# Optimization experiments

Measured on AMD Instinct MI355X. Metric: run time of the kernel, lower is better.

The kernel has to match this reference:

```python
import math
import numpy as np
import jax, jax.numpy as jnp

C = 8  # hidden multiplicity (num_channels)
B, N = 4, 4096

# ---------- real Wigner 3j (e3nn convention: Frobenius norm 1) ----------

def _su2_cg(l1, l2, l3):
    f = math.factorial
    def cg(m1, m2, m3):
        if m1 + m2 != m3:
            return 0.0
        pref = math.sqrt((2 * l3 + 1) * f(l3 + l1 - l2) * f(l3 - l1 + l2) * f(l1 + l2 - l3) / f(l1 + l2 + l3 + 1))
        pref *= math.sqrt(f(l3 + m3) * f(l3 - m3) * f(l1 - m1) * f(l1 + m1) * f(l2 - m2) * f(l2 + m2))
        s = 0.0
        for k in range(l1 + l2 - l3 + 1):
            d = [k, l1 + l2 - l3 - k, l1 - m1 - k, l2 + m2 - k, l3 - l2 + m1 + k, l3 - l1 - m2 + k]
            if min(d) < 0:
                continue
            s += (-1.0) ** k / np.prod([float(f(x)) for x in d])
        return pref * s
    out = np.zeros((2 * l1 + 1, 2 * l2 + 1, 2 * l3 + 1))
    for i, m1 in enumerate(range(-l1, l1 + 1)):
        for j, m2 in enumerate(range(-l2, l2 + 1)):
            for k, m3 in enumerate(range(-l3, l3 + 1)):
                out[i, j, k] = cg(m1, m2, m3)
    return out

def _q_real_to_complex(l):
    q = np.zeros((2 * l + 1, 2 * l + 1), dtype=np.complex128)
    rs2 = 1.0 / math.sqrt(2.0)
    for m in range(-l, 0):
        q[l + m, l + abs(m)] = rs2
        q[l + m, l - abs(m)] = -1j * rs2
    q[l, l] = 1.0
    for m in range(1, l + 1):
        q[l + m, l + abs(m)] = (-1) ** m * rs2
        q[l + m, l - abs(m)] = 1j * (-1) ** m * rs2
    return (-1j) ** l * q

def _w3j(l1, l2, l3):
    Q1, Q2, Q3 = _q_real_to_complex(l1), _q_real_to_complex(l2), _q_real_to_complex(l3)
    Cc = _su2_cg(l1, l2, l3).astype(np.complex128)
    Cr = np.real(np.einsum('ij,kl,mn,ikm->jln', Q1, Q2, np.conj(Q3), Cc))
    return (Cr / np.linalg.norm(Cr)).astype(np.float32)

# tensor-product paths (selection rules for 4e/6e inputs, 0e/2e SH, 4e/6e outputs)
VAL_PATHS = [(4, 0, 4), (4, 2, 4), (6, 2, 4), (4, 2, 6), (6, 0, 6), (6, 2, 6)]
OUT_PATHS = [(4, 4, 4), (4, 6, 4), (6, 4, 4), (6, 6, 4), (4, 4, 6), (4, 6, 6), (6, 4, 6), (6, 6, 6)]
# path normalization ('element'): fan-in = 3*C for tp_val outputs, 4*C^2 for tp_out outputs
W3J_VAL = [jnp.asarray(_w3j(*p) * math.sqrt((2 * p[2] + 1) / (3.0 * C))) for p in VAL_PATHS]
W3J_OUT = [jnp.asarray(_w3j(*p) * math.sqrt((2 * p[2] + 1) / (4.0 * C * C))) for p in OUT_PATHS]


def _forward(feat, sh_lr, log_s, pos_w, pos_b, w_lin_in, w_val, w_out, w_lin_out):
    b, n, _ = feat.shape
    f4, f6 = feat[..., :9], feat[..., 9:]                      # 1x4e, 1x6e
    f4n = f4 / jnp.maximum(jnp.linalg.norm(f4, axis=-1, keepdims=True), 1e-12)
    f6n = f6 / jnp.maximum(jnp.linalg.norm(f6, axis=-1, keepdims=True), 1e-12)
    s4, s6 = jnp.exp(log_s[0]), jnp.exp(log_s[1])
    scores = s4 * jnp.einsum('bnd,bmd->bnm', f4n, f4n) + s6 * jnp.einsum('bnd,bmd->bnm', f6n, f6n)
    pb = sh_lr @ pos_w + pos_b                                 # (N,)
    scores = scores + (pb[:, None] + pb[None, :])[None]
    attn = jax.nn.softmax(scores.astype(jnp.float32), axis=-1).astype(feat.dtype)

    h4 = f4[:, :, None, :] * w_lin_in[0][None, None, :, None]  # (B,N,C,9)
    h6 = f6[:, :, None, :] * w_lin_in[1][None, None, :, None]  # (B,N,C,13)

    y = {0: sh_lr[:, :1], 2: sh_lr[:, 1:]}                     # (N,1), (N,5)
    hx = {4: h4, 6: h6}
    v = {4: jnp.zeros((b, n, C, 9), feat.dtype), 6: jnp.zeros((b, n, C, 13), feat.dtype)}
    for p, (l1, l2, l3) in enumerate(VAL_PATHS):
        v[l3] = v[l3] + jnp.einsum('bnui,nj,ijk,uw->bnwk', hx[l1], y[l2], W3J_VAL[p], w_val[p])
    vals = jnp.concatenate([v[4].reshape(b, n, 9 * C), v[6].reshape(b, n, 13 * C)], axis=-1)

    ctx = jnp.einsum('bnm,bmd->bnd', attn, vals)               # (B,N,22C)
    cx = {4: ctx[..., :9 * C].reshape(b, n, C, 9), 6: ctx[..., 9 * C:].reshape(b, n, C, 13)}
    o = {4: jnp.zeros((b, n, C, 9), feat.dtype), 6: jnp.zeros((b, n, C, 13), feat.dtype)}
    for p, (l1, l2, l3) in enumerate(OUT_PATHS):
        o[l3] = o[l3] + jnp.einsum('bnui,bnvj,ijk,uvw->bnwk', hx[l1], cx[l2], W3J_OUT[p], w_out[p])

    inv_sc = 1.0 / math.sqrt(C)                                # lin_out fan_in = C
    d4 = jnp.einsum('bnui,u->bni', o[4], w_lin_out[0]) * inv_sc
    d6 = jnp.einsum('bnui,u->bni', o[6], w_lin_out[1]) * inv_sc
    return jnp.concatenate([d4, d6], axis=-1)                  # (B,N,22)


def setup_inputs() -> dict:
    key = jax.random.key(0)
    ks = jax.random.split(key, 8)
    feat = jax.random.normal(ks[0], (B, N, 22), jnp.float32)
    sh_lr = jax.random.normal(ks[1], (N, 6), jnp.float32)
    log_s = jnp.array([math.log(1.0 / 3.0), math.log(1.0 / math.sqrt(13.0))], jnp.float32)
    pos_w = 0.01 * jax.random.normal(ks[2], (6,), jnp.float32)
    pos_b = jnp.zeros((), jnp.float32)
    w_lin_in = jax.random.normal(ks[3], (2, C), jnp.float32)
    w_val = jax.random.normal(ks[4], (6, C, C), jnp.float32)
    w_out = jax.random.normal(ks[5], (8, C, C, C), jnp.float32)
    w_lin_out = jax.random.normal(ks[6], (2, C), jnp.float32)
    return dict(feat=feat, sh_lr=sh_lr, log_s=log_s, pos_w=pos_w, pos_b=pos_b,
                w_lin_in=w_lin_in, w_val=w_val, w_out=w_out, w_lin_out=w_lin_out)


def reference(feat, sh_lr, log_s, pos_w, pos_b, w_lin_in, w_val, w_out, w_lin_out):
    return _forward(feat, sh_lr, log_s, pos_w, pos_b, w_lin_in, w_val, w_out, w_lin_out)
```

## Files before the change

kernel.cpp:

```cpp
#include <hip/hip_runtime.h>
#include <cmath>

#define NN 4096
#define BB 4
#define CCH 8

#define OFF_W3JVAL 0
#define OFF_W3JOUT 2688
#define OFF_CTX0   13568
#define CTXS       1572864
#define OFFB_KGH   25220096ULL
#define OFFB_KGL   26268672ULL
#define OFFB_VG    27317248ULL
#define OFFB_WBH   30462976ULL
#define OFFB_WBL   30493696ULL

typedef short s16x8 __attribute__((ext_vector_type(8)));
typedef _Float16 f16x8 __attribute__((ext_vector_type(8)));
typedef float f32x4 __attribute__((ext_vector_type(4)));
typedef unsigned int u32x4 __attribute__((ext_vector_type(4)));
typedef unsigned int u32x2 __attribute__((ext_vector_type(2)));

static __device__ __forceinline__ unsigned short f2bf(float x){
  unsigned u = __float_as_uint(x);
  return (unsigned short)((u + 0x7FFFu + ((u >> 16) & 1u)) >> 16);
}
static __device__ __forceinline__ float bf2f(unsigned short h){
  return __uint_as_float(((unsigned)h) << 16);
}
static __device__ __forceinline__ unsigned pk2r(float v){
  unsigned short h = f2bf(v);
  unsigned short l = f2bf(v - bf2f(h));
  return ((unsigned)l << 16) | (unsigned)h;
}
static __device__ __forceinline__ unsigned short f2h(float x){
  return __builtin_bit_cast(unsigned short, (_Float16)x);
}
static __device__ __forceinline__ void unpk(u32x4 a, u32x4 b, s16x8& h, s16x8& l){
  u32x4 hw = { __builtin_amdgcn_perm(a[1],a[0],0x05040100u),
               __builtin_amdgcn_perm(a[3],a[2],0x05040100u),
               __builtin_amdgcn_perm(b[1],b[0],0x05040100u),
               __builtin_amdgcn_perm(b[3],b[2],0x05040100u)};
  u32x4 lw = { __builtin_amdgcn_perm(a[1],a[0],0x07060302u),
               __builtin_amdgcn_perm(a[3],a[2],0x07060302u),
               __builtin_amdgcn_perm(b[1],b[0],0x07060302u),
               __builtin_amdgcn_perm(b[3],b[2],0x07060302u)};
  h = __builtin_bit_cast(s16x8, hw);
  l = __builtin_bit_cast(s16x8, lw);
}
static __device__ __forceinline__ void barrier_lds(){
  __asm__ volatile("s_waitcnt lgkmcnt(0)\n\ts_barrier" ::: "memory");
}

static __device__ __forceinline__ void qentf(int l, int r, int c, float& re, float& im){
  re=0.f; im=0.f;
  float s = ((l&3)==2)? -1.f : 1.f;
  const float rs2 = 0.70710678118654752440f;
  if(r < l){
    if(c == 2*l - r) re = s*rs2;
    else if(c == r)  im = -s*rs2;
  } else if(r == l){
    if(c == l) re = s;
  } else {
    float sg = ((r-l)&1)? -1.f : 1.f;
    if(c == r) re = s*sg*rs2;
    else if(c == 2*l - r) im = s*sg*rs2;
  }
}
__global__ __launch_bounds__(256) void k_tab(float* __restrict__ Wv, float* __restrict__ Wo){
  __shared__ float Ccf[2197];
  __shared__ float red[256];
  __shared__ double factS[20];
  int t = threadIdx.x;
  int p = blockIdx.x;
  if(t==0){
    double f=1.0; factS[0]=1.0;
    for(int i=1;i<20;i++){ f*=(double)i; factS[i]=f; }
  }
  const int L1[14]={4,4,6,4,6,6, 4,4,6,6,4,4,6,6};
  const int L2[14]={0,2,2,2,0,2, 4,6,4,6,4,6,4,6};
  const int L3[14]={4,4,4,6,6,6, 4,4,4,4,6,6,6,6};
  const int OFF[14]={0,81,486,1071,1656,1825, 0,729,1782,2835,4356,5409,6930,8451};
  int l1=L1[p], l2=L2[p], l3=L3[p];
  int d1=2*l1+1, d2=2*l2+1, d3=2*l3+1;
  int tot = d1*d2*d3;
  float* dst = (p<6) ? (Wv+OFF[p]) : (Wo+OFF[p]);
  float scale = (p<6) ? sqrtf((2.f*l3+1.f)/24.f) : sqrtf((2.f*l3+1.f)/256.f);
  __syncthreads();
  #pragma unroll 1
  for(int e=t; e<tot; e+=256){
    int i = e/(d2*d3), rem = e - i*(d2*d3), j = rem/d3, k = rem - j*d3;
    int m1=i-l1, m2=j-l2, m3=k-l3;
    double v=0.0;
    if(m1+m2==m3){
      double pref = sqrt((2.0*l3+1.0)*factS[l3+l1-l2]*factS[l3-l1+l2]*factS[l1+l2-l3]/factS[l1+l2+l3+1]);
      pref *= sqrt(factS[l3+m3]*factS[l3-m3]*factS[l1-m1]*factS[l1+m1]*factS[l2-m2]*factS[l2+m2]);
      double s=0.0;
      #pragma unroll 1
      for(int kk=0; kk<=l1+l2-l3; kk++){
        int dd0=kk, dd1=l1+l2-l3-kk, dd2=l1-m1-kk, dd3=l2+m2-kk, dd4=l3-l2+m1+kk, dd5=l3-l1-m2+kk;
        int mn=dd0;
        if(dd1<mn)mn=dd1; if(dd2<mn)mn=dd2; if(dd3<mn)mn=dd3; if(dd4<mn)mn=dd4; if(dd5<mn)mn=dd5;
        if(mn<0) continue;
        double prod = factS[dd0]*factS[dd1]*factS[dd2]*factS[dd3]*factS[dd4]*factS[dd5];
        s += ((kk&1)? -1.0:1.0)/prod;
      }
      v = pref*s;
    }
    Ccf[e]=(float)v;
  }
  __syncthreads();
  float nacc=0.f;
  #pragma unroll 1
  for(int e=t; e<tot; e+=256){
    int j = e/(d2*d3), rem = e - j*(d2*d3), l = rem/d3, n = rem - l*d3;
    float re = 0.f;
    #pragma unroll
    for(int ii=0; ii<2; ii++){
      int i = ii ? (2*l1 - j) : j;
      float q1r,q1i; qentf(l1,i,j,q1r,q1i);
      if(ii && i==j){ q1r=0.f; q1i=0.f; }
      #pragma unroll
      for(int kk=0; kk<2; kk++){
        int k = kk ? (2*l2 - l) : l;
        float q2r,q2i; qentf(l2,k,l,q2r,q2i);
        if(kk && k==l){ q2r=0.f; q2i=0.f; }
        float ar = q1r*q2r - q1i*q2i;
        float ai = q1r*q2i + q1i*q2r;
        #pragma unroll
        for(int mm=0; mm<2; mm++){
          int m = mm ? (2*l3 - n) : n;
          float q3r,q3i; qentf(l3,m,n,q3r,q3i);
          if(mm && m==n){ q3r=0.f; q3i=0.f; }
          float coef = ar*q3r + ai*q3i;
          re = fmaf(coef, Ccf[(i*d2+k)*d3+m], re);
        }
      }
    }
    dst[e]=re;
    nacc = fmaf(re,re,nacc);
  }
  red[t]=nacc;
  __syncthreads();
  #pragma unroll 1
  for(int s=128;s>0;s>>=1){
    if(t<s) red[t]+=red[t+s];
    __syncthreads();
  }
  float c = scale/sqrtf(red[0]);
  #pragma unroll 1
  for(int e=t; e<tot; e+=256) dst[e]*=c;
}

__global__ void k_weights(const float* __restrict__ wli, const float* __restrict__ wval,
                          const float* __restrict__ wout, const float* __restrict__ wlo,
                          const float* __restrict__ Wv,
                          unsigned short* __restrict__ WBH, unsigned short* __restrict__ WBL){
  __shared__ float bws[48];
  __shared__ float scs[64];
  __shared__ float As[24];
  int t = threadIdx.x;
  if(t<48){
    const int val_l1[6]={0,0,1,0,1,1};
    int p=t>>3, w=t&7;
    float s=0.f;
    for(int u=0;u<8;u++) s = fmaf(wli[val_l1[p]*8+u], wval[(p*8+u)*8+w], s);
    bws[t]=s;
  }
  {
    const int out_l1[8]={0,0,1,1,0,0,1,1};
    const int out_l3[8]={0,0,0,0,1,1,1,1};
    int p=t>>3, v=t&7;
    float s=0.f;
    for(int u=0;u<8;u++){
      float a=wli[out_l1[p]*8+u];
      for(int w=0;w<8;w++) s = fmaf(wout[((p*8+u)*8+v)*8+w]*a, wlo[out_l3[p]*8+w], s);
    }
    scs[t]=s*0.35355339059327373f;
  }
  __syncthreads();
  if(t<24){
    int p=t/3, i3=t-3*p;
    int vp = (p&1)*3 + i3;
    float s=0.f;
    for(int w=0;w<8;w++) s = fmaf(scs[p*8+w], bws[vp*8+w], s);
    As[t]=s;
  }
  __syncthreads();
  int base = blockIdx.x*960;
  for(int k=0;k<15;k++){
    int cell = base + k*64 + t;
    int f = cell/160, c = cell - f*160;
    float v = 0.f;
    if(f < 88 && c < 132){
      int seg = f/22, off = f - seg*22;
      int even = (off < 9);
      int p = 2*seg + (even?0:1);
      int jo = even ? off : off-9;
      int l1, i, jj;
      if(c < 54){ l1=4; i=c/6; jj=c-6*i; }
      else { int cc=c-54; l1=6; i=cc/6; jj=cc-6*i; }
      if(even){
        if(l1==4 && jj==0)      v = As[p*3+0]*Wv[i*9+jo];
        else if(l1==4)          v = As[p*3+1]*Wv[81+(i*5+jj-1)*9+jo];
        else if(jj>=1)          v = As[p*3+2]*Wv[486+(i*5+jj-1)*9+jo];
      } else {
        if(l1==4 && jj>=1)      v = As[p*3+0]*Wv[1071+(i*5+jj-1)*13+jo];
        else if(l1==6 && jj==0) v = As[p*3+1]*Wv[1656+i*13+jo];
        else if(l1==6)          v = As[p*3+2]*Wv[1825+(i*5+jj-1)*13+jo];
      }
    } else if(f==88 && c==132){
      v = 1.0f;
    }
    unsigned short h = f2bf(v);
    WBH[cell] = h;
    WBL[cell] = f2bf(v - bf2f(h));
  }
}

__launch_bounds__(128)
__global__ void k_prep(const float* __restrict__ feat, const float* __restrict__ sh,
                       const float* __restrict__ log_s, const float* __restrict__ pos_w,
                       const float* __restrict__ pos_b,
                       const unsigned short* __restrict__ WBH,
                       const unsigned short* __restrict__ WBL,
                       unsigned short* __restrict__ Kgh, unsigned short* __restrict__ Kgl,
                       unsigned short* __restrict__ Vg){
  __shared__ __align__(16) unsigned int Pbuf[16*164];
  __shared__ unsigned int Po[96*17];
  __shared__ float epbs[16];
  int tid = threadIdx.x;
  int w2 = tid >> 6, lane = tid & 63;
  int lm = lane & 15, quad = lane >> 4;
  int seg = w2*4 + quad;
  int panel = blockIdx.x >> 2, mt = blockIdx.x & 3;
  int idxp = panel*64 + mt*16 + lm;
  int n = idxp & (NN-1);
  const float* fp = feat + (size_t)idxp*22;
  const float* shp = sh + n*6;
  float f[22];
  #pragma unroll
  for(int c=0;c<22;c++) f[c]=fp[c];
  float y[6];
  #pragma unroll
  for(int j=0;j<6;j++) y[j]=shp[j];
  if(tid<16){
    float pb = pos_b[0];
    #pragma unroll
    for(int j=0;j<6;j++) pb = fmaf(y[j], pos_w[j], pb);
    epbs[lm] = __expf(pb);
    float n4=0.f, n6=0.f;
    #pragma unroll
    for(int c=0;c<9;c++) n4 += f[c]*f[c];
    #pragma unroll
    for(int c=9;c<22;c++) n6 += f[c]*f[c];
    n4 = fmaxf(sqrtf(n4), 1e-12f);
    n6 = fmaxf(sqrtf(n6), 1e-12f);
    float s4 = __expf(log_s[0]), s6 = __expf(log_s[1]);
    float a4 = sqrtf(s4)/n4, a6 = sqrtf(s6)/n6;
    unsigned short* kph = Kgh + (size_t)idxp*32;
    unsigned short* kpl = Kgl + (size_t)idxp*32;
    #pragma unroll
    for(int c=0;c<22;c++){
      float qv = f[c] * (c<9 ? a4 : a6);
      unsigned short h = f2bf(qv);
      kph[c]=h; kpl[c]=f2bf(qv - bf2f(h));
    }
    #pragma unroll
    for(int c=22;c<32;c++){ kph[c]=0; kpl[c]=0; }
  }
  #pragma unroll
  for(int j4=0;j4<5;j4++){
    u32x4 wv;
    #pragma unroll
    for(int e=0;e<4;e++){
      int c = seg*20 + j4*4 + e;
      float pv;
      if(c<54){ int i=c/6, jj=c-6*i; pv = f[i]*y[jj]; }
      else if(c<132){ int cc=c-54; int i=cc/6, jj=cc-6*i; pv = f[9+i]*y[jj]; }
      else if(c==132) pv = 1.0f;
      else pv = 0.0f;
      wv[e] = pk2r(pv);
    }
    *(u32x4*)&Pbuf[lm*164 + seg*20 + j4*4] = wv;
  }
  __syncthreads();
  f32x4 acc[3];
  #pragma unroll
  for(int ft=0;ft<3;ft++)
    #pragma unroll
    for(int i=0;i<4;i++) acc[ft][i]=0.f;
  for(int kc=0;kc<5;kc++){
    const u32x4* ap = (const u32x4*)&Pbuf[lm*164 + kc*32 + quad*8];
    s16x8 Ah, Al;
    unpk(ap[0], ap[1], Ah, Al);
    #pragma unroll
    for(int ft=0;ft<3;ft++){
      int ftg = w2*3 + ft;
      size_t bo = (size_t)(ftg*16+lm)*160 + kc*32 + quad*8;
      s16x8 Bh = *(const s16x8*)(WBH + bo);
      s16x8 Bl = *(const s16x8*)(WBL + bo);
      f32x4 a = acc[ft];
      a = __builtin_amdgcn_mfma_f32_16x16x32_bf16(Al, Bl, a, 0,0,0);
      a = __builtin_amdgcn_mfma_f32_16x16x32_bf16(Al, Bh, a, 0,0,0);
      a = __builtin_amdgcn_mfma_f32_16x16x32_bf16(Ah, Bl, a, 0,0,0);
      a = __builtin_amdgcn_mfma_f32_16x16x32_bf16(Ah, Bh, a, 0,0,0);
      acc[ft] = a;
    }
  }
  #pragma unroll
  for(int r=0;r<4;r++){
    float e = epbs[quad*4 + r];
    #pragma unroll
    for(int ft=0;ft<3;ft++){
      int ftg = w2*3 + ft;
      Po[(ftg*16+lm)*17 + quad*4 + r] = (unsigned)f2h(acc[ft][r]*e);
    }
  }
  __syncthreads();
  unsigned int* vO32 = (unsigned int*)(Vg + (size_t)panel*96*64);
  #pragma unroll
  for(int wv=0; wv<6; wv++){
    int idx2 = wv*128 + tid;
    int g = idx2 >> 3, j = idx2 & 7;
    unsigned lo = Po[g*17 + 2*j] & 0xFFFFu;
    unsigned hi = Po[g*17 + 2*j + 1] & 0xFFFFu;
    vO32[g*32 + mt*8 + j] = lo | (hi<<16);
  }
}

#define ESB 16384
__global__ __launch_bounds__(512)
__attribute__((amdgpu_waves_per_eu(4, 4)))
void k_attn(const unsigned short* __restrict__ Kgh,
            const unsigned short* __restrict__ Kgl,
            const unsigned short* __restrict__ Vg,
            float* __restrict__ ctx0){
  __shared__ __align__(16) unsigned char Es[2][ESB];
  int tid = threadIdx.x;
  int lane = tid & 63, w = tid >> 6;
  int lm = lane & 15, quad = lane >> 4;
  int blk = blockIdx.x;
  int b = blk & 3, hd = (blk>>2)&3, qb = blk >> 4;
  int qrow0 = qb * 128;
  const unsigned short* KhB = Kgh + (size_t)b*NN*32;
  const unsigned short* KlB = Kgl + (size_t)b*NN*32;
  const unsigned short* VB  = Vg  + (size_t)b*64*96*64;
  float* ctx = ctx0 + (size_t)hd*CTXS + (size_t)b*NN*96;

  int sq = w & 3;
  int sk = w >> 2;

  s16x8 qh[2], ql[2];
  #pragma unroll
  for(int q2=0;q2<2;q2++){
    size_t ro = (size_t)(qrow0 + (2*sq+q2)*16 + lm)*32 + (size_t)quad*8;
    qh[q2] = *(const s16x8*)(KhB + ro);
    ql[q2] = *(const s16x8*)(KlB + ro);
  }
  int wofs[2][2], rofs[2][2];
  #pragma unroll
  for(int q2=0;q2<2;q2++){
    int row = (2*sq+q2)*16 + lm;
    int xo = (row & 7) << 4;
    #pragma unroll
    for(int k2=0;k2<2;k2++)
      wofs[k2][q2] = row*128 + ((((2*sk+k2)*32) + quad*8) ^ xo);
    #pragma unroll
    for(int ks=0;ks<2;ks++)
      rofs[ks][q2] = row*128 + (((ks*64) + quad*16) ^ xo);
  }

  f32x4 acc[2][3];
  #pragma unroll
  for(int q2=0;q2<2;q2++)
    #pragma unroll
    for(int ft=0;ft<3;ft++)
      #pragma unroll
      for(int i=0;i<4;i++) acc[q2][ft][i]=0.f;

  s16x8 kh_[2][2], kl_[2][2];
  f16x8 vv[2][3];

#define MFB(A,Bv,C) __builtin_amdgcn_mfma_f32_16x16x32_bf16(A,Bv,C,0,0,0)
#define MFH(A,Bv,C) __builtin_amdgcn_mfma_f32_16x16x32_f16(A,Bv,C,0,0,0)

#define LOADK(T,Bk) { size_t pk_ = (size_t)(hd*16+(T))*2048; \
  _Pragma("unroll") \
  for(int k2=0;k2<2;k2++){ \
    size_t ko_ = pk_ + (size_t)((2*sk+k2)*16+lm)*32 + (size_t)(quad*8); \
    kh_[Bk][k2] = *(const s16x8*)(KhB + ko_); \
    kl_[Bk][k2] = *(const s16x8*)(KlB + ko_); } }

#define LOADV(T) { size_t pv_ = (size_t)(hd*16+(T))*6144; \
  _Pragma("unroll") \
  for(int ks=0;ks<2;ks++) \
  _Pragma("unroll") \
  for(int ft=0;ft<3;ft++){ \
    size_t vo_ = pv_ + (size_t)((3*sk+ft)*16+lm)*64 + (size_t)(ks*32+quad*8); \
    vv[ks][ft] = *(const f16x8*)(VB + vo_); } }

#define SPH(Bk,CUR) { \
  _Pragma("unroll") \
  for(int k2=0;k2<2;k2++) \
  _Pragma("unroll") \
  for(int q2=0;q2<2;q2++){ \
    f32x4 s_ = {0.f,0.f,0.f,0.f}; \
    s_ = MFB(kl_[Bk][k2], qh[q2], s_); \
    s_ = MFB(kh_[Bk][k2], ql[q2], s_); \
    s_ = MFB(kh_[Bk][k2], qh[q2], s_); \
    unsigned u01_ = (unsigned)f2h(__expf(s_[0])) | ((unsigned)f2h(__expf(s_[1]))<<16); \
    unsigned u23_ = (unsigned)f2h(__expf(s_[2])) | ((unsigned)f2h(__expf(s_[3]))<<16); \
    *(u32x2*)&Es[CUR][wofs[k2][q2]] = (u32x2){u01_, u23_}; } }

#define PVH(PRV) { \
  _Pragma("unroll") \
  for(int ks=0;ks<2;ks++) \
  _Pragma("unroll") \
  for(int q2=0;q2<2;q2++){ \
    f16x8 e_ = *(const f16x8*)&Es[PRV][rofs[ks][q2]]; \
    _Pragma("unroll") \
    for(int ft=0;ft<3;ft++) \
      acc[q2][ft] = MFH(e_, vv[ks][ft], acc[q2][ft]); } }

  LOADK(0,0);
  LOADV(0);
  LOADK(1,1);
  SPH(0,0);
  barrier_lds();

  #pragma unroll 1
  for(int t=1; t<14; t+=2){
    LOADK(t+1,0);
    PVH(0);
    LOADV(t);
    SPH(1,1);
    barrier_lds();
    LOADK(t+2,1);
    PVH(1);
    LOADV(t+1);
    SPH(0,0);
    barrier_lds();
  }
  PVH(0);
  LOADV(15);
  SPH(1,1);
  barrier_lds();
  PVH(1);

#undef MFB
#undef MFH
#undef LOADK
#undef LOADV
#undef SPH
#undef PVH

  #pragma unroll
  for(int q2=0;q2<2;q2++){
    #pragma unroll
    for(int ft=0;ft<3;ft++){
      int col = (3*sk+ft)*16 + lm;
      #pragma unroll
      for(int r=0;r<4;r++){
        int row = qrow0 + (2*sq+q2)*16 + quad*4 + r;
        ctx[(size_t)row*96 + col] = acc[q2][ft][r];
      }
    }
  }
}

__launch_bounds__(256, 2)
__global__ void k_out(const float* __restrict__ feat, const float* __restrict__ ctxA,
                      const float* __restrict__ w3jout, float* __restrict__ out){
  __shared__ float gbuf[64*45];
  __shared__ float fbuf[64*24];
  __shared__ float dls[4*64*13];
  __shared__ float inv[64];
  int tid = threadIdx.x;
  int typ = blockIdx.x & 1;
  int n0 = (blockIdx.x>>1)*64;
  int gc0 = typ*44;
  for(int i=tid;i<64*44;i+=256){
    int pt=i/44, c=i-pt*44;
    const float* base = ctxA + (size_t)(n0+pt)*96 + gc0 + c;
    gbuf[pt*45+c] = base[0]+base[CTXS]+base[2*CTXS]+base[3*CTXS];
  }
  for(int i=tid;i<64*22;i+=256){
    int pt=i/22, c=i-pt*22;
    fbuf[pt*24+c] = feat[(size_t)(n0+pt)*22+c];
  }
  if(tid<64){
    const float* bd = ctxA + (size_t)(n0+tid)*96 + 88;
    inv[tid] = 1.0f/(bd[0]+bd[CTXS]+bd[2*CTXS]+bd[3*CTXS]);
  }
  __syncthreads();
  int lane = tid&63, w = tid>>6;
  float fR[13], gR[13], d[13];
  {
    int FB = (w&2)?9:0;
    int fn = (w&2)?13:9;
    #pragma unroll 13
    for(int i=0;i<13;i++) fR[i] = (i<fn) ? fbuf[lane*24 + FB + i] : 0.f;
    int GBl = (w==0)?0:(w==1)?9:(w==2)?22:31;
    int jn = (w&1)?13:9;
    #pragma unroll 13
    for(int j=0;j<13;j++) gR[j] = (j<jn) ? gbuf[lane*45 + GBl + j] : 0.f;
  }
  #pragma unroll 13
  for(int k=0;k<13;k++) d[k]=0.f;

#define PATHR(ID,JD,KD,WO) \
  _Pragma("unroll") \
  for(int i=0;i<(ID);i++){ float fv=fR[i]; \
    _Pragma("unroll") \
    for(int j=0;j<(JD);j++){ float val=fv*gR[j]; \
      const float* wp = w3jout + (WO) + (i*(JD)+j)*(KD); \
      _Pragma("unroll") \
      for(int k=0;k<(KD);k++) d[k] = fmaf(val, wp[k], d[k]); } }

  int pcase = typ*4 + w;
  switch(pcase){
    case 0: PATHR(9,9,9, 0)       break;
    case 1: PATHR(9,13,9, 729)    break;
    case 2: PATHR(13,9,9, 1782)   break;
    case 3: PATHR(13,13,9, 2835)  break;
    case 4: PATHR(9,9,13, 4356)   break;
    case 5: PATHR(9,13,13, 5409)  break;
    case 6: PATHR(13,9,13, 6930)  break;
    default:PATHR(13,13,13, 8451) break;
  }
#undef PATHR
  {
    float* dp = &dls[(w*64+lane)*13];
    #pragma unroll 13
    for(int k=0;k<13;k++) dp[k]=d[k];
  }
  __syncthreads();
  {
    int KD = typ?13:9;
    int kb = typ?9:0;
    int pt = tid&63, kc = tid>>6;
    float iv = inv[pt];
    #pragma unroll
    for(int e=0;e<4;e++){
      int k = kc*4+e;
      if(k<KD){
        float s = dls[(0*64+pt)*13+k] + dls[(1*64+pt)*13+k]
                + dls[(2*64+pt)*13+k] + dls[(3*64+pt)*13+k];
        out[(size_t)(n0+pt)*22 + kb + k] = s*iv;
      }
    }
  }
}

extern "C" void kernel_launch(void* const* d_in, const int* in_sizes, int n_in,
                              void* d_out, int out_size, void* d_ws, size_t ws_size,
                              hipStream_t stream){
  (void)in_sizes; (void)n_in; (void)out_size; (void)ws_size;
  const float* feat =(const float*)d_in[0];
  const float* sh   =(const float*)d_in[1];
  const float* log_s=(const float*)d_in[2];
  const float* pos_w=(const float*)d_in[3];
  const float* pos_b=(const float*)d_in[4];
  const float* wli  =(const float*)d_in[5];
  const float* wval =(const float*)d_in[6];
  const float* wout =(const float*)d_in[7];
  const float* wlo  =(const float*)d_in[8];
  float* outp=(float*)d_out;
  float* wsf=(float*)d_ws;

  unsigned short* Kgh=(unsigned short*)((char*)d_ws + OFFB_KGH);
  unsigned short* Kgl=(unsigned short*)((char*)d_ws + OFFB_KGL);
  unsigned short* Vg =(unsigned short*)((char*)d_ws + OFFB_VG);
  unsigned short* WBH=(unsigned short*)((char*)d_ws + OFFB_WBH);
  unsigned short* WBL=(unsigned short*)((char*)d_ws + OFFB_WBL);

  hipLaunchKernelGGL(k_tab, dim3(14), dim3(256), 0, stream,
                     wsf+OFF_W3JVAL, wsf+OFF_W3JOUT);
  hipLaunchKernelGGL(k_weights, dim3(16), dim3(64), 0, stream,
                     wli, wval, wout, wlo, wsf+OFF_W3JVAL, WBH, WBL);
  hipLaunchKernelGGL(k_prep, dim3(1024), dim3(128), 0, stream,
                     feat, sh, log_s, pos_w, pos_b, WBH, WBL,
                     Kgh, Kgl, Vg);
  hipLaunchKernelGGL(k_attn, dim3(512), dim3(512), 0, stream,
                     Kgh, Kgl, Vg, wsf+OFF_CTX0);
  hipLaunchKernelGGL(k_out, dim3(512), dim3(256), 0, stream,
                     feat, wsf+OFF_CTX0, wsf+OFF_W3JOUT, outp);
}
```

Baseline: 216.8 us.

## Stage K/V tiles in LDS and keep attention weights in registers via bpermute

Restructures the attention kernel so each wave owns 16 query rows and all 96 output columns. K-hi, K-lo and V tiles are cooperatively loaded into double-buffered LDS instead of each wave reading them straight from global memory. The exp-score tile is no longer written to and re-read from LDS; it is redistributed across lanes with ds_bpermute and fed directly into the f16 MFMA. This cuts redundant global loads and the LDS round-trip for probabilities, but raises LDS use to 72KB per block and adds bpermute and selection overhead.

```diff
diff --git a/kernel.cpp b/kernel.cpp
--- a/kernel.cpp
+++ b/kernel.cpp
@@ -47,9 +47,6 @@
                __builtin_amdgcn_perm(b[3],b[2],0x07060302u)};
   h = __builtin_bit_cast(s16x8, hw);
   l = __builtin_bit_cast(s16x8, lw);
-}
-static __device__ __forceinline__ void barrier_lds(){
-  __asm__ volatile("s_waitcnt lgkmcnt(0)\n\ts_barrier" ::: "memory");
 }
 
 static __device__ __forceinline__ void qentf(int l, int r, int c, float& re, float& im){
@@ -329,142 +326,140 @@
   }
 }
 
-#define ESB 16384
+#define LDSK  0
+#define LDSKL 4096
+#define LDSV  8192
+#define BUFB  20480
 __global__ __launch_bounds__(512)
 __attribute__((amdgpu_waves_per_eu(4, 4)))
 void k_attn(const unsigned short* __restrict__ Kgh,
             const unsigned short* __restrict__ Kgl,
             const unsigned short* __restrict__ Vg,
             float* __restrict__ ctx0){
-  __shared__ __align__(16) unsigned char Es[2][ESB];
+  __shared__ __align__(16) unsigned char lds[73728];
   int tid = threadIdx.x;
   int lane = tid & 63, w = tid >> 6;
   int lm = lane & 15, quad = lane >> 4;
   int blk = blockIdx.x;
-  int b = blk & 3, hd = (blk>>2)&3, qb = blk >> 4;
-  int qrow0 = qb * 128;
+  int b = blk & 3, kh = (blk>>2)&3, qb = blk >> 4;
   const unsigned short* KhB = Kgh + (size_t)b*NN*32;
   const unsigned short* KlB = Kgl + (size_t)b*NN*32;
   const unsigned short* VB  = Vg  + (size_t)b*64*96*64;
-  float* ctx = ctx0 + (size_t)hd*CTXS + (size_t)b*NN*96;
-
-  int sq = w & 3;
-  int sk = w >> 2;
-
-  s16x8 qh[2], ql[2];
-  #pragma unroll
-  for(int q2=0;q2<2;q2++){
-    size_t ro = (size_t)(qrow0 + (2*sq+q2)*16 + lm)*32 + (size_t)quad*8;
-    qh[q2] = *(const s16x8*)(KhB + ro);
-    ql[q2] = *(const s16x8*)(KlB + ro);
-  }
-  int wofs[2][2], rofs[2][2];
-  #pragma unroll
-  for(int q2=0;q2<2;q2++){
-    int row = (2*sq+q2)*16 + lm;
-    int xo = (row & 7) << 4;
-    #pragma unroll
-    for(int k2=0;k2<2;k2++)
-      wofs[k2][q2] = row*128 + ((((2*sk+k2)*32) + quad*8) ^ xo);
-    #pragma unroll
-    for(int ks=0;ks<2;ks++)
-      rofs[ks][q2] = row*128 + (((ks*64) + quad*16) ^ xo);
-  }
-
-  f32x4 acc[2][3];
-  #pragma unroll
-  for(int q2=0;q2<2;q2++)
-    #pragma unroll
-    for(int ft=0;ft<3;ft++)
-      #pragma unroll
-      for(int i=0;i<4;i++) acc[q2][ft][i]=0.f;
-
-  s16x8 kh_[2][2], kl_[2][2];
-  f16x8 vv[2][3];
+  float* ctx = ctx0 + (size_t)kh*CTXS + (size_t)b*NN*96;
+  int qrow = qb*128 + w*16 + lm;
+
+  s16x8 qh, ql;
+  { size_t ro = (size_t)qrow*32 + (size_t)quad*8;
+    qh = *(const s16x8*)(KhB + ro);
+    ql = *(const s16x8*)(KlB + ro); }
+
+  int kro = lm*64 + ((quad ^ ((lm>>1)&3))<<4);
+  int vr0 = lm*128 + (((0*4+quad) ^ (lm&7))<<4);
+  int vr1 = lm*128 + (((1*4+quad) ^ (lm&7))<<4);
+  int bpa0 = (lm + 16*((quad&1)*2 + 0))<<2;
+  int bpa1 = (lm + 16*((quad&1)*2 + 1))<<2;
+  bool hiq = (quad >= 2);
+
+  int dofs[3], sofs[3], sreg[3];
+  #pragma unroll
+  for(int rep=0;rep<3;rep++){
+    int g = tid + 512*rep;
+    if(g < 256){ sreg[rep]=0; sofs[rep]=g*16;
+      dofs[rep] = LDSK + (g>>2)*64 + (((g&3) ^ ((g>>3)&3))<<4); }
+    else if(g < 512){ int g2=g-256; sreg[rep]=1; sofs[rep]=g2*16;
+      dofs[rep] = LDSKL + (g2>>2)*64 + (((g2&3) ^ ((g2>>3)&3))<<4); }
+    else if(g < 1280){ int gv=g-512; sreg[rep]=2; sofs[rep]=gv*16;
+      dofs[rep] = LDSV + (gv>>3)*128 + (((gv&7) ^ ((gv>>3)&7))<<4); }
+    else { sreg[rep]=-1; sofs[rep]=0; dofs[rep]=0; }
+  }
+
+  f32x4 acc[6];
+  #pragma unroll
+  for(int ft=0;ft<6;ft++)
+    #pragma unroll
+    for(int i=0;i<4;i++) acc[ft][i]=0.f;
+
+  u32x4 stg0, stg1, stg2;
 
 #define MFB(A,Bv,C) __builtin_amdgcn_mfma_f32_16x16x32_bf16(A,Bv,C,0,0,0)
 #define MFH(A,Bv,C) __builtin_amdgcn_mfma_f32_16x16x32_f16(A,Bv,C,0,0,0)
 
-#define LOADK(T,Bk) { size_t pk_ = (size_t)(hd*16+(T))*2048; \
+#define STG_ISSUE(T) { \
+  const char* kb_ = (const char*)(KhB + (size_t)(kh*16+(T))*2048); \
+  const char* lb_ = (const char*)(KlB + (size_t)(kh*16+(T))*2048); \
+  const char* vb_ = (const char*)(VB  + (size_t)(kh*16+(T))*6144); \
+  { const char* sp_ = (sreg[0]==0)? kb_ : (sreg[0]==1)? lb_ : vb_; \
+    stg0 = *(const u32x4*)(sp_ + sofs[0]); } \
+  { const char* sp_ = (sreg[1]==0)? kb_ : (sreg[1]==1)? lb_ : vb_; \
+    stg1 = *(const u32x4*)(sp_ + sofs[1]); } \
+  if(sreg[2]>=0){ stg2 = *(const u32x4*)(vb_ + sofs[2]); } }
+
+#define STG_WRITE(BN) { \
+  *(u32x4*)&lds[(BN)*BUFB + dofs[0]] = stg0; \
+  *(u32x4*)&lds[(BN)*BUFB + dofs[1]] = stg1; \
+  if(sreg[2]>=0){ *(u32x4*)&lds[(BN)*BUFB + dofs[2]] = stg2; } }
+
+#define COMPUTE(B) { \
+  unsigned Wt[4][2]; \
   _Pragma("unroll") \
-  for(int k2=0;k2<2;k2++){ \
-    size_t ko_ = pk_ + (size_t)((2*sk+k2)*16+lm)*32 + (size_t)(quad*8); \
-    kh_[Bk][k2] = *(const s16x8*)(KhB + ko_); \
-    kl_[Bk][k2] = *(const s16x8*)(KlB + ko_); } }
-
-#define LOADV(T) { size_t pv_ = (size_t)(hd*16+(T))*6144; \
+  for(int kt=0;kt<4;kt++){ \
+    s16x8 kfh = *(const s16x8*)&lds[(B)*BUFB + LDSK  + kt*1024 + kro]; \
+    s16x8 kfl = *(const s16x8*)&lds[(B)*BUFB + LDSKL + kt*1024 + kro]; \
+    f32x4 s_ = {0.f,0.f,0.f,0.f}; \
+    s_ = MFB(kfl, qh, s_); \
+    s_ = MFB(kfh, ql, s_); \
+    s_ = MFB(kfh, qh, s_); \
+    Wt[kt][0] = (unsigned)f2h(__expf(s_[0])) | ((unsigned)f2h(__expf(s_[1]))<<16); \
+    Wt[kt][1] = (unsigned)f2h(__expf(s_[2])) | ((unsigned)f2h(__expf(s_[3]))<<16); \
+  } \
   _Pragma("unroll") \
-  for(int ks=0;ks<2;ks++) \
-  _Pragma("unroll") \
-  for(int ft=0;ft<3;ft++){ \
-    size_t vo_ = pv_ + (size_t)((3*sk+ft)*16+lm)*64 + (size_t)(ks*32+quad*8); \
-    vv[ks][ft] = *(const f16x8*)(VB + vo_); } }
-
-#define SPH(Bk,CUR) { \
-  _Pragma("unroll") \
-  for(int k2=0;k2<2;k2++) \
-  _Pragma("unroll") \
-  for(int q2=0;q2<2;q2++){ \
-    f32x4 s_ = {0.f,0.f,0.f,0.f}; \
-    s_ = MFB(kl_[Bk][k2], qh[q2], s_); \
-    s_ = MFB(kh_[Bk][k2], ql[q2], s_); \
-    s_ = MFB(kh_[Bk][k2], qh[q2], s_); \
-    unsigned u01_ = (unsigned)f2h(__expf(s_[0])) | ((unsigned)f2h(__expf(s_[1]))<<16); \
-    unsigned u23_ = (unsigned)f2h(__expf(s_[2])) | ((unsigned)f2h(__expf(s_[3]))<<16); \
-    *(u32x2*)&Es[CUR][wofs[k2][q2]] = (u32x2){u01_, u23_}; } }
-
-#define PVH(PRV) { \
-  _Pragma("unroll") \
-  for(int ks=0;ks<2;ks++) \
-  _Pragma("unroll") \
-  for(int q2=0;q2<2;q2++){ \
-    f16x8 e_ = *(const f16x8*)&Es[PRV][rofs[ks][q2]]; \
+  for(int c=0;c<2;c++){ \
+    unsigned pa[4]; \
     _Pragma("unroll") \
-    for(int ft=0;ft<3;ft++) \
-      acc[q2][ft] = MFH(e_, vv[ks][ft], acc[q2][ft]); } }
-
-  LOADK(0,0);
-  LOADV(0);
-  LOADK(1,1);
-  SPH(0,0);
-  barrier_lds();
+    for(int i=0;i<4;i++){ \
+      int ad_ = (i<2) ? bpa0 : bpa1; \
+      int a0_ = __builtin_amdgcn_ds_bpermute(ad_, (int)Wt[2*c  ][i&1]); \
+      int a1_ = __builtin_amdgcn_ds_bpermute(ad_, (int)Wt[2*c+1][i&1]); \
+      pa[i] = hiq ? (unsigned)a1_ : (unsigned)a0_; } \
+    u32x4 paw = {pa[0],pa[1],pa[2],pa[3]}; \
+    f16x8 PA = __builtin_bit_cast(f16x8, paw); \
+    int vro_ = c ? vr1 : vr0; \
+    _Pragma("unroll") \
+    for(int ft=0;ft<6;ft++){ \
+      f16x8 vf = *(const f16x8*)&lds[(B)*BUFB + LDSV + ft*2048 + vro_]; \
+      acc[ft] = MFH(PA, vf, acc[ft]); } \
+  } }
+
+  STG_ISSUE(0);
+  STG_WRITE(0);
+  __syncthreads();
 
   #pragma unroll 1
-  for(int t=1; t<14; t+=2){
-    LOADK(t+1,0);
-    PVH(0);
-    LOADV(t);
-    SPH(1,1);
-    barrier_lds();
-    LOADK(t+2,1);
-    PVH(1);
-    LOADV(t+1);
-    SPH(0,0);
-    barrier_lds();
-  }
-  PVH(0);
-  LOADV(15);
-  SPH(1,1);
-  barrier_lds();
-  PVH(1);
+  for(int tp=0; tp<8; tp++){
+    int t0 = 2*tp;
+    STG_ISSUE(t0+1);
+    COMPUTE(0);
+    STG_WRITE(1);
+    __syncthreads();
+    if(t0+2 < 16){ STG_ISSUE(t0+2); }
+    COMPUTE(1);
+    if(t0+2 < 16){ STG_WRITE(0); }
+    __syncthreads();
+  }
 
 #undef MFB
 #undef MFH
-#undef LOADK
-#undef LOADV
-#undef SPH
-#undef PVH
-
-  #pragma unroll
-  for(int q2=0;q2<2;q2++){
-    #pragma unroll
-    for(int ft=0;ft<3;ft++){
-      int col = (3*sk+ft)*16 + lm;
-      #pragma unroll
-      for(int r=0;r<4;r++){
-        int row = qrow0 + (2*sq+q2)*16 + quad*4 + r;
-        ctx[(size_t)row*96 + col] = acc[q2][ft][r];
-      }
+#undef STG_ISSUE
+#undef STG_WRITE
+#undef COMPUTE
+
+  #pragma unroll
+  for(int ft=0;ft<6;ft++){
+    int col = ft*16 + lm;
+    #pragma unroll
+    for(int r=0;r<4;r++){
+      int row = qb*128 + w*16 + quad*4 + r;
+      ctx[(size_t)row*96 + col] = acc[ft][r];
     }
   }
 }
```

Measured after the change: 194.4 us. 1.12x faster.
